# Performance work log

Hardware: AMD Instinct MI355X
Metric: run time of the kernel (lower is better)

## Reference

```python
import jax, jax.numpy as jnp
import numpy as np
from jax import lax

BCE_WEIGHT = 0.5
DICE_WEIGHT = 0.5
BOUNDARY_WEIGHT = 3.0
KERNEL_SIZE = 3
SMOOTH = 1e-6
EPS = 1e-7  # clamp for log stability (torch BCE clamps log at -100)


def setup_inputs() -> dict:
    key = jax.random.key(0)
    k1, k2 = jax.random.split(key)
    B, C, H, W = 32, 1, 512, 512
    pred = jax.random.uniform(k1, (B, C, H, W), dtype=jnp.float32)
    target = jax.random.randint(k2, (B, C, H, W), 0, 2, dtype=jnp.int32)
    return {"pred": pred, "target": target}


def _extract_boundary(t):
    # cv2 dilate/erode with all-ones 3x3 kernel == 3x3 max/min pooling.
    # cv2 morphology border behavior (-inf for dilate, +inf for erode)
    # matches reduce_window identity padding with 'SAME'.
    k = KERNEL_SIZE
    win = (1, 1, k, k)
    one = (1, 1, 1, 1)
    dilated = lax.reduce_window(t, -jnp.inf, lax.max, win, one, 'SAME')
    eroded = lax.reduce_window(t, jnp.inf, lax.min, win, one, 'SAME')
    return dilated - eroded  # in {0,1} for binary masks


def reference(pred, target):
    t = target.astype(jnp.float32)  # (B,1,H,W) binary

    # Boundary-aware weighted BCE
    boundary = _extract_boundary(t)
    weights = jnp.where(boundary > 0, BOUNDARY_WEIGHT, 1.0)
    p = jnp.clip(pred, EPS, 1.0 - EPS)
    bce_map = -(t * jnp.log(p) + (1.0 - t) * jnp.log1p(-p))
    bce = jnp.mean(bce_map * weights)

    # Dice loss over flattened tensors
    pf = pred.reshape(-1)
    tf = t.reshape(-1)
    intersection = jnp.sum(pf * tf)
    dice_coef = (2.0 * intersection + SMOOTH) / (jnp.sum(pf) + jnp.sum(tf) + SMOOTH)
    dice = 1.0 - dice_coef

    total = BCE_WEIGHT * bce + DICE_WEIGHT * dice
    return total, bce, dice
```

## Files before the change

kernel.cpp:

```cpp
#include <hip/hip_runtime.h>


#define BB 32
#define HH 512
#define WW 512
#define N_TOTAL (BB * HH * WW)
#define SEG 8
#define W8 (WW / SEG)
#define NSEG (BB * HH * W8)
#define NBLK 2048

__global__ __launch_bounds__(256) void loss_main_kernel(
        const float* __restrict__ pred,
        const int* __restrict__ target,
        double* __restrict__ partials) {
    float wbce = 0.f, inter = 0.f, sp = 0.f;
    int st_i = 0;

    const int lane = threadIdx.x & 63;
    const int stride = gridDim.x * blockDim.x;
    for (int seg = blockIdx.x * blockDim.x + threadIdx.x; seg < NSEG;
         seg += stride) {
        const int w0 = (seg & (W8 - 1)) << 3;
        const int h  = (seg >> 6) & (HH - 1);
        const int b  = seg >> 15;

        const size_t rowbase = ((size_t)(b * HH + h)) * WW;

        const float4 p0 = *(const float4*)(pred + rowbase + w0);
        const float4 p1 = *(const float4*)(pred + rowbase + w0 + 4);

        const int* rowC = target + rowbase;
        const int* rowU = (h > 0)      ? rowC - WW : rowC;
        const int* rowD = (h < HH - 1) ? rowC + WW : rowC;

        const int4 uA = *(const int4*)(rowU + w0);
        const int4 uB = *(const int4*)(rowU + w0 + 4);
        const int4 cA = *(const int4*)(rowC + w0);
        const int4 cB = *(const int4*)(rowC + w0 + 4);
        const int4 dA = *(const int4*)(rowD + w0);
        const int4 dB = *(const int4*)(rowD + w0 + 4);

        const int o0 = uA.x | cA.x | dA.x,  n0 = uA.x & cA.x & dA.x;
        const int o1 = uA.y | cA.y | dA.y,  n1 = uA.y & cA.y & dA.y;
        const int o2 = uA.z | cA.z | dA.z,  n2 = uA.z & cA.z & dA.z;
        const int o3 = uA.w | cA.w | dA.w,  n3 = uA.w & cA.w & dA.w;
        const int o4 = uB.x | cB.x | dB.x,  n4 = uB.x & cB.x & dB.x;
        const int o5 = uB.y | cB.y | dB.y,  n5 = uB.y & cB.y & dB.y;
        const int o6 = uB.z | cB.z | dB.z,  n6 = uB.z & cB.z & dB.z;
        const int o7 = uB.w | cB.w | dB.w,  n7 = uB.w & cB.w & dB.w;

        int oL = __shfl_up(o7, 1);
        int nL = __shfl_up(n7, 1);
        int oR = __shfl_down(o0, 1);
        int nR = __shfl_down(n0, 1);
        if (lane == 0)  { oL = o0; nL = n0; }
        if (lane == 63) { oR = o7; nR = n7; }

        const int e0 = (oL | o0 | o1) != (nL & n0 & n1);
        const int e1 = (o0 | o1 | o2) != (n0 & n1 & n2);
        const int e2 = (o1 | o2 | o3) != (n1 & n2 & n3);
        const int e3 = (o2 | o3 | o4) != (n2 & n3 & n4);
        const int e4 = (o3 | o4 | o5) != (n3 & n4 & n5);
        const int e5 = (o4 | o5 | o6) != (n4 & n5 & n6);
        const int e6 = (o5 | o6 | o7) != (n5 & n6 & n7);
        const int e7 = (o6 | o7 | oR) != (n6 & n7 & nR);

#define ACC(T, P, E)                                                   \
        {                                                              \
            const float pc = fminf(fmaxf((P), 1e-7f), 1.0f - 1e-7f);   \
            const float x  = (T) ? pc : (1.0f - pc);                   \
            wbce += ((E) ? 3.0f : 1.0f) * (-__logf(x));                \
            sp += (P);                                                 \
            if (T) inter += (P);                                       \
            st_i += (T);                                               \
        }

        ACC(cA.x, p0.x, e0); ACC(cA.y, p0.y, e1);
        ACC(cA.z, p0.z, e2); ACC(cA.w, p0.w, e3);
        ACC(cB.x, p1.x, e4); ACC(cB.y, p1.y, e5);
        ACC(cB.z, p1.z, e6); ACC(cB.w, p1.w, e7);
#undef ACC
    }

    float st = (float)st_i;
    #pragma unroll
    for (int off = 32; off > 0; off >>= 1) {
        wbce  += __shfl_down(wbce,  off);
        inter += __shfl_down(inter, off);
        sp    += __shfl_down(sp,    off);
        st    += __shfl_down(st,    off);
    }

    __shared__ float smem[4][4];
    const int wave = threadIdx.x >> 6;
    if ((threadIdx.x & 63) == 0) {
        smem[wave][0] = wbce; smem[wave][1] = inter;
        smem[wave][2] = sp;   smem[wave][3] = st;
    }
    __syncthreads();
    if (threadIdx.x == 0) {
        float a0 = 0, a1 = 0, a2 = 0, a3 = 0;
        #pragma unroll
        for (int wv = 0; wv < 4; ++wv) {
            a0 += smem[wv][0]; a1 += smem[wv][1];
            a2 += smem[wv][2]; a3 += smem[wv][3];
        }
        double* dst = partials + (size_t)blockIdx.x * 4;
        dst[0] = (double)a0; dst[1] = (double)a1;
        dst[2] = (double)a2; dst[3] = (double)a3;
    }
}

__global__ __launch_bounds__(256) void finalize_kernel(
        const double* __restrict__ partials, float* __restrict__ out) {
    double a0 = 0, a1 = 0, a2 = 0, a3 = 0;
    #pragma unroll
    for (int k = 0; k < NBLK / 256; ++k) {
        const double* src = partials + (size_t)(k * 256 + threadIdx.x) * 4;
        a0 += src[0]; a1 += src[1]; a2 += src[2]; a3 += src[3];
    }
    #pragma unroll
    for (int off = 32; off > 0; off >>= 1) {
        a0 += __shfl_down(a0, off);
        a1 += __shfl_down(a1, off);
        a2 += __shfl_down(a2, off);
        a3 += __shfl_down(a3, off);
    }
    __shared__ double smem[4][4];
    const int wave = threadIdx.x >> 6;
    if ((threadIdx.x & 63) == 0) {
        smem[wave][0] = a0; smem[wave][1] = a1;
        smem[wave][2] = a2; smem[wave][3] = a3;
    }
    __syncthreads();
    if (threadIdx.x == 0) {
        double s0 = 0, s1 = 0, s2 = 0, s3 = 0;
        #pragma unroll
        for (int wv = 0; wv < 4; ++wv) {
            s0 += smem[wv][0]; s1 += smem[wv][1];
            s2 += smem[wv][2]; s3 += smem[wv][3];
        }
        const double bce = s0 / (double)N_TOTAL;
        const double dice_coef = (2.0 * s1 + 1e-6) / (s2 + s3 + 1e-6);
        const double dice = 1.0 - dice_coef;
        const double total = 0.5 * bce + 0.5 * dice;
        out[0] = (float)total;
        out[1] = (float)bce;
        out[2] = (float)dice;
    }
}

extern "C" void kernel_launch(void* const* d_in, const int* in_sizes, int n_in,
                              void* d_out, int out_size, void* d_ws, size_t ws_size,
                              hipStream_t stream) {
    const float* pred  = (const float*)d_in[0];
    const int* target  = (const int*)d_in[1];
    float* out = (float*)d_out;
    double* partials = (double*)d_ws;

    loss_main_kernel<<<NBLK, 256, 0, stream>>>(pred, target, partials);
    finalize_kernel<<<1, 256, 0, stream>>>(partials, out);
}
```

Measured before the change: 21.85 us.

## Process two rows per wave to reuse halo target rows, drop grid-stride loop

Each wave now handles two adjacent image rows, loading four target rows instead of three per output row, so the vertical 3x3 neighbourhood is shared between the two rows. The grid-stride loop is removed; every thread handles one 2x8 tile exactly once. Block partials are stored as a float4 instead of four doubles, and the finalize kernel uses 1024 threads. The trade-off is less per-thread memory-level parallelism from the loop, and float partials give slightly lower precision.

```diff
diff --git a/kernel.cpp b/kernel.cpp
--- a/kernel.cpp
+++ b/kernel.cpp
@@ -5,83 +5,99 @@
 #define HH 512
 #define WW 512
 #define N_TOTAL (BB * HH * WW)
-#define SEG 8
-#define W8 (WW / SEG)
-#define NSEG (BB * HH * W8)
 #define NBLK 2048
 
 __global__ __launch_bounds__(256) void loss_main_kernel(
         const float* __restrict__ pred,
         const int* __restrict__ target,
-        double* __restrict__ partials) {
+        float4* __restrict__ partials) {
+    const int wave = threadIdx.x >> 6;
+    const int lane = threadIdx.x & 63;
+    const int gw   = blockIdx.x * 4 + wave;
+    const int b    = gw >> 8;
+    const int h0   = (gw & 255) << 1;
+    const int w0   = lane << 3;
+
+    const size_t img = (size_t)b * (HH * WW);
+    const int* tg   = target + img;
+    const float* pg = pred + img;
+
+    const int hm = (h0 > 0) ? h0 - 1 : 0;
+    const int hp = (h0 + 2 < HH) ? h0 + 2 : HH - 1;
+
+    const int4 r0A = *(const int4*)(tg + (size_t)hm * WW + w0);
+    const int4 r0B = *(const int4*)(tg + (size_t)hm * WW + w0 + 4);
+    const int4 r1A = *(const int4*)(tg + (size_t)h0 * WW + w0);
+    const int4 r1B = *(const int4*)(tg + (size_t)h0 * WW + w0 + 4);
+    const int4 r2A = *(const int4*)(tg + (size_t)(h0 + 1) * WW + w0);
+    const int4 r2B = *(const int4*)(tg + (size_t)(h0 + 1) * WW + w0 + 4);
+    const int4 r3A = *(const int4*)(tg + (size_t)hp * WW + w0);
+    const int4 r3B = *(const int4*)(tg + (size_t)hp * WW + w0 + 4);
+
+    const float4 pT0 = *(const float4*)(pg + (size_t)h0 * WW + w0);
+    const float4 pT1 = *(const float4*)(pg + (size_t)h0 * WW + w0 + 4);
+    const float4 pB0 = *(const float4*)(pg + (size_t)(h0 + 1) * WW + w0);
+    const float4 pB1 = *(const float4*)(pg + (size_t)(h0 + 1) * WW + w0 + 4);
+
+#define VC(i, u, c1, c2, d)                                          \
+    const int so##i = (c1) | (c2), sa##i = (c1) & (c2);              \
+    const int oT##i = so##i | (u), nT##i = sa##i & (u);              \
+    const int oB##i = so##i | (d), nB##i = sa##i & (d);
+    VC(0, r0A.x, r1A.x, r2A.x, r3A.x)
+    VC(1, r0A.y, r1A.y, r2A.y, r3A.y)
+    VC(2, r0A.z, r1A.z, r2A.z, r3A.z)
+    VC(3, r0A.w, r1A.w, r2A.w, r3A.w)
+    VC(4, r0B.x, r1B.x, r2B.x, r3B.x)
+    VC(5, r0B.y, r1B.y, r2B.y, r3B.y)
+    VC(6, r0B.z, r1B.z, r2B.z, r3B.z)
+    VC(7, r0B.w, r1B.w, r2B.w, r3B.w)
+#undef VC
+
+    int oTL = __shfl_up(oT7, 1),   nTL = __shfl_up(nT7, 1);
+    int oTR = __shfl_down(oT0, 1), nTR = __shfl_down(nT0, 1);
+    int oBL = __shfl_up(oB7, 1),   nBL = __shfl_up(nB7, 1);
+    int oBR = __shfl_down(oB0, 1), nBR = __shfl_down(nB0, 1);
+    if (lane == 0)  { oTL = oT0; nTL = nT0; oBL = oB0; nBL = nB0; }
+    if (lane == 63) { oTR = oT7; nTR = nT7; oBR = oB7; nBR = nB7; }
+
+    const int eT0 = (oTL | oT0 | oT1) != (nTL & nT0 & nT1);
+    const int eT1 = (oT0 | oT1 | oT2) != (nT0 & nT1 & nT2);
+    const int eT2 = (oT1 | oT2 | oT3) != (nT1 & nT2 & nT3);
+    const int eT3 = (oT2 | oT3 | oT4) != (nT2 & nT3 & nT4);
+    const int eT4 = (oT3 | oT4 | oT5) != (nT3 & nT4 & nT5);
+    const int eT5 = (oT4 | oT5 | oT6) != (nT4 & nT5 & nT6);
+    const int eT6 = (oT5 | oT6 | oT7) != (nT5 & nT6 & nT7);
+    const int eT7 = (oT6 | oT7 | oTR) != (nT6 & nT7 & nTR);
+    const int eB0 = (oBL | oB0 | oB1) != (nBL & nB0 & nB1);
+    const int eB1 = (oB0 | oB1 | oB2) != (nB0 & nB1 & nB2);
+    const int eB2 = (oB1 | oB2 | oB3) != (nB1 & nB2 & nB3);
+    const int eB3 = (oB2 | oB3 | oB4) != (nB2 & nB3 & nB4);
+    const int eB4 = (oB3 | oB4 | oB5) != (nB3 & nB4 & nB5);
+    const int eB5 = (oB4 | oB5 | oB6) != (nB4 & nB5 & nB6);
+    const int eB6 = (oB5 | oB6 | oB7) != (nB5 & nB6 & nB7);
+    const int eB7 = (oB6 | oB7 | oBR) != (nB6 & nB7 & nBR);
+
     float wbce = 0.f, inter = 0.f, sp = 0.f;
     int st_i = 0;
 
-    const int lane = threadIdx.x & 63;
-    const int stride = gridDim.x * blockDim.x;
-    for (int seg = blockIdx.x * blockDim.x + threadIdx.x; seg < NSEG;
-         seg += stride) {
-        const int w0 = (seg & (W8 - 1)) << 3;
-        const int h  = (seg >> 6) & (HH - 1);
-        const int b  = seg >> 15;
-
-        const size_t rowbase = ((size_t)(b * HH + h)) * WW;
-
-        const float4 p0 = *(const float4*)(pred + rowbase + w0);
-        const float4 p1 = *(const float4*)(pred + rowbase + w0 + 4);
-
-        const int* rowC = target + rowbase;
-        const int* rowU = (h > 0)      ? rowC - WW : rowC;
-        const int* rowD = (h < HH - 1) ? rowC + WW : rowC;
-
-        const int4 uA = *(const int4*)(rowU + w0);
-        const int4 uB = *(const int4*)(rowU + w0 + 4);
-        const int4 cA = *(const int4*)(rowC + w0);
-        const int4 cB = *(const int4*)(rowC + w0 + 4);
-        const int4 dA = *(const int4*)(rowD + w0);
-        const int4 dB = *(const int4*)(rowD + w0 + 4);
-
-        const int o0 = uA.x | cA.x | dA.x,  n0 = uA.x & cA.x & dA.x;
-        const int o1 = uA.y | cA.y | dA.y,  n1 = uA.y & cA.y & dA.y;
-        const int o2 = uA.z | cA.z | dA.z,  n2 = uA.z & cA.z & dA.z;
-        const int o3 = uA.w | cA.w | dA.w,  n3 = uA.w & cA.w & dA.w;
-        const int o4 = uB.x | cB.x | dB.x,  n4 = uB.x & cB.x & dB.x;
-        const int o5 = uB.y | cB.y | dB.y,  n5 = uB.y & cB.y & dB.y;
-        const int o6 = uB.z | cB.z | dB.z,  n6 = uB.z & cB.z & dB.z;
-        const int o7 = uB.w | cB.w | dB.w,  n7 = uB.w & cB.w & dB.w;
-
-        int oL = __shfl_up(o7, 1);
-        int nL = __shfl_up(n7, 1);
-        int oR = __shfl_down(o0, 1);
-        int nR = __shfl_down(n0, 1);
-        if (lane == 0)  { oL = o0; nL = n0; }
-        if (lane == 63) { oR = o7; nR = n7; }
-
-        const int e0 = (oL | o0 | o1) != (nL & n0 & n1);
-        const int e1 = (o0 | o1 | o2) != (n0 & n1 & n2);
-        const int e2 = (o1 | o2 | o3) != (n1 & n2 & n3);
-        const int e3 = (o2 | o3 | o4) != (n2 & n3 & n4);
-        const int e4 = (o3 | o4 | o5) != (n3 & n4 & n5);
-        const int e5 = (o4 | o5 | o6) != (n4 & n5 & n6);
-        const int e6 = (o5 | o6 | o7) != (n5 & n6 & n7);
-        const int e7 = (o6 | o7 | oR) != (n6 & n7 & nR);
-
 #define ACC(T, P, E)                                                   \
-        {                                                              \
-            const float pc = fminf(fmaxf((P), 1e-7f), 1.0f - 1e-7f);   \
-            const float x  = (T) ? pc : (1.0f - pc);                   \
-            wbce += ((E) ? 3.0f : 1.0f) * (-__logf(x));                \
-            sp += (P);                                                 \
-            if (T) inter += (P);                                       \
-            st_i += (T);                                               \
-        }
-
-        ACC(cA.x, p0.x, e0); ACC(cA.y, p0.y, e1);
-        ACC(cA.z, p0.z, e2); ACC(cA.w, p0.w, e3);
-        ACC(cB.x, p1.x, e4); ACC(cB.y, p1.y, e5);
-        ACC(cB.z, p1.z, e6); ACC(cB.w, p1.w, e7);
+    {                                                                  \
+        const float pc = fminf(fmaxf((P), 1e-7f), 1.0f - 1e-7f);       \
+        const float x  = (T) ? pc : (1.0f - pc);                       \
+        wbce += ((E) ? 3.0f : 1.0f) * (-__logf(x));                    \
+        sp += (P);                                                     \
+        if (T) inter += (P);                                           \
+        st_i += (T);                                                   \
+    }
+    ACC(r1A.x, pT0.x, eT0); ACC(r1A.y, pT0.y, eT1);
+    ACC(r1A.z, pT0.z, eT2); ACC(r1A.w, pT0.w, eT3);
+    ACC(r1B.x, pT1.x, eT4); ACC(r1B.y, pT1.y, eT5);
+    ACC(r1B.z, pT1.z, eT6); ACC(r1B.w, pT1.w, eT7);
+    ACC(r2A.x, pB0.x, eB0); ACC(r2A.y, pB0.y, eB1);
+    ACC(r2A.z, pB0.z, eB2); ACC(r2A.w, pB0.w, eB3);
+    ACC(r2B.x, pB1.x, eB4); ACC(r2B.y, pB1.y, eB5);
+    ACC(r2B.z, pB1.z, eB6); ACC(r2B.w, pB1.w, eB7);
 #undef ACC
-    }
 
     float st = (float)st_i;
     #pragma unroll
@@ -93,32 +109,29 @@
     }
 
     __shared__ float smem[4][4];
-    const int wave = threadIdx.x >> 6;
     if ((threadIdx.x & 63) == 0) {
         smem[wave][0] = wbce; smem[wave][1] = inter;
         smem[wave][2] = sp;   smem[wave][3] = st;
     }
     __syncthreads();
     if (threadIdx.x == 0) {
-        float a0 = 0, a1 = 0, a2 = 0, a3 = 0;
+        float s0 = 0, s1 = 0, s2 = 0, s3 = 0;
         #pragma unroll
         for (int wv = 0; wv < 4; ++wv) {
-            a0 += smem[wv][0]; a1 += smem[wv][1];
-            a2 += smem[wv][2]; a3 += smem[wv][3];
+            s0 += smem[wv][0]; s1 += smem[wv][1];
+            s2 += smem[wv][2]; s3 += smem[wv][3];
         }
-        double* dst = partials + (size_t)blockIdx.x * 4;
-        dst[0] = (double)a0; dst[1] = (double)a1;
-        dst[2] = (double)a2; dst[3] = (double)a3;
+        partials[blockIdx.x] = make_float4(s0, s1, s2, s3);
     }
 }
 
-__global__ __launch_bounds__(256) void finalize_kernel(
-        const double* __restrict__ partials, float* __restrict__ out) {
+__global__ __launch_bounds__(1024) void finalize_kernel(
+        const float4* __restrict__ partials, float* __restrict__ out) {
     double a0 = 0, a1 = 0, a2 = 0, a3 = 0;
     #pragma unroll
-    for (int k = 0; k < NBLK / 256; ++k) {
-        const double* src = partials + (size_t)(k * 256 + threadIdx.x) * 4;
-        a0 += src[0]; a1 += src[1]; a2 += src[2]; a3 += src[3];
+    for (int k = 0; k < NBLK / 1024; ++k) {
+        const float4 p = partials[k * 1024 + threadIdx.x];
+        a0 += p.x; a1 += p.y; a2 += p.z; a3 += p.w;
     }
     #pragma unroll
     for (int off = 32; off > 0; off >>= 1) {
@@ -127,7 +140,7 @@
         a2 += __shfl_down(a2, off);
         a3 += __shfl_down(a3, off);
     }
-    __shared__ double smem[4][4];
+    __shared__ double smem[16][4];
     const int wave = threadIdx.x >> 6;
     if ((threadIdx.x & 63) == 0) {
         smem[wave][0] = a0; smem[wave][1] = a1;
@@ -137,7 +150,7 @@
     if (threadIdx.x == 0) {
         double s0 = 0, s1 = 0, s2 = 0, s3 = 0;
         #pragma unroll
-        for (int wv = 0; wv < 4; ++wv) {
+        for (int wv = 0; wv < 16; ++wv) {
             s0 += smem[wv][0]; s1 += smem[wv][1];
             s2 += smem[wv][2]; s3 += smem[wv][3];
         }
@@ -157,8 +170,8 @@
     const float* pred  = (const float*)d_in[0];
     const int* target  = (const int*)d_in[1];
     float* out = (float*)d_out;
-    double* partials = (double*)d_ws;
+    float4* partials = (float4*)d_ws;
 
     loss_main_kernel<<<NBLK, 256, 0, stream>>>(pred, target, partials);
-    finalize_kernel<<<1, 256, 0, stream>>>(partials, out);
+    finalize_kernel<<<1, 1024, 0, stream>>>(partials, out);
 }
```

Measured after the change: 22.01 us. About the same (+0.7%).
